# Optimization experiments

Hardware: AMD Instinct MI355X
Metric: run time of the kernel (lower is better)

Reference implementation:

```python
import jax, jax.numpy as jnp
import numpy as np

HEADS = 4
KS = 7          # neighborhood kernel size
EPS = 1e-5
C = 64
N, H, W = 8, 64, 64


def _gather_idx(L, k):
    # NATTEN-style neighborhood: window centered at pixel, shifted to stay in bounds.
    start = jnp.clip(jnp.arange(L) - k // 2, 0, L - k)            # [L]
    idx = start[:, None] + jnp.arange(k)                           # [L, k] absolute neighbor idx
    # relative-position-bias index: (query - neighbor) + (k-1) in [0, 2k-2]
    rel = (jnp.arange(L) - start)[:, None] + (k - 1) - jnp.arange(k)[None, :]  # [L, k]
    return idx, rel


def na2d(x, qkv_w, qkv_b, rpb, proj_w, proj_b):
    # x: [N, H, W, C] -> neighborhood attention with rel-pos bias
    n, h, w, c = x.shape
    hd = c // HEADS
    scale = hd ** -0.5
    qkv = (x @ qkv_w.T + qkv_b).reshape(n, h, w, 3, HEADS, hd)
    q = qkv[..., 0, :, :] * scale                                  # [n,h,w,heads,hd]
    k = qkv[..., 1, :, :]
    v = qkv[..., 2, :, :]
    idx_h, rel_h = _gather_idx(h, KS)
    idx_w, rel_w = _gather_idx(w, KS)
    # gather neighborhoods: [n, h, k, w, k, heads, hd]
    kg = k[:, idx_h][:, :, :, idx_w]
    vg = v[:, idx_h][:, :, :, idx_w]
    attn = jnp.einsum('nijhd,niajbhd->nijhab', q, kg)              # [n,h,w,heads,k,k]
    bias = rpb[:, rel_h, :]                                        # [heads, h, k, 2k-1]
    bias = jnp.take(bias, rel_w, axis=-1)                          # [heads, h, k, w, k]
    bias = jnp.transpose(bias, (1, 3, 0, 2, 4))                    # [h, w, heads, k, k]
    attn = attn + bias
    a = jax.nn.softmax(attn.reshape(n, h, w, HEADS, KS * KS), axis=-1).reshape(attn.shape)
    out = jnp.einsum('nijhab,niajbhd->nijhd', a, vg).reshape(n, h, w, c)
    return out @ proj_w.T + proj_b


def setup_inputs() -> dict:
    key = jax.random.key(0)
    ks = jax.random.split(key, 12)
    s = 0.02
    return {
        'x': jax.random.normal(ks[0], (N, C, H, W), jnp.float32),
        'gn_w': jnp.ones((C,), jnp.float32),
        'gn_b': jnp.zeros((C,), jnp.float32),
        'qkv_w': jax.random.normal(ks[1], (3 * C, C), jnp.float32) * s,
        'qkv_b': jnp.zeros((3 * C,), jnp.float32),
        'rpb': jax.random.normal(ks[2], (HEADS, 2 * KS - 1, 2 * KS - 1), jnp.float32) * s,
        'proj_w': jax.random.normal(ks[3], (C, C), jnp.float32) * s,
        'proj_b': jnp.zeros((C,), jnp.float32),
        'ln_w': jnp.ones((C,), jnp.float32),
        'ln_b': jnp.zeros((C,), jnp.float32),
        'fc1_w': jax.random.normal(ks[4], (4 * C, C), jnp.float32) * s,
        'fc1_b': jnp.zeros((4 * C,), jnp.float32),
        'fc2_w': jax.random.normal(ks[5], (C, 4 * C), jnp.float32) * s,
        'fc2_b': jnp.zeros((C,), jnp.float32),
    }


def reference(x, gn_w, gn_b, qkv_w, qkv_b, rpb, proj_w, proj_b,
              ln_w, ln_b, fc1_w, fc1_b, fc2_w, fc2_b):
    n, c, h, w = x.shape
    x1 = jnp.transpose(x, (0, 2, 3, 1))                            # residual, NHWC
    # GroupNorm(1, C): normalize over (C,H,W) per sample, per-channel affine
    mu = jnp.mean(x, axis=(1, 2, 3), keepdims=True)
    var = jnp.var(x, axis=(1, 2, 3), keepdims=True)
    xg = (x - mu) * jax.lax.rsqrt(var + EPS)
    xg = xg * gn_w[None, :, None, None] + gn_b[None, :, None, None]
    xg = jnp.transpose(xg, (0, 2, 3, 1))                           # NHWC
    y = na2d(xg, qkv_w, qkv_b, rpb, proj_w, proj_b) + x1           # [n,h,w,c]
    y = y.reshape(n, h * w, c)
    # LayerNorm over channels + MLP (GELU), residual
    mu2 = jnp.mean(y, axis=-1, keepdims=True)
    var2 = jnp.var(y, axis=-1, keepdims=True)
    yn = (y - mu2) * jax.lax.rsqrt(var2 + EPS) * ln_w + ln_b
    hdn = jax.nn.gelu(yn @ fc1_w.T + fc1_b, approximate=False)
    y = y + (hdn @ fc2_w.T + fc2_b)
    return jnp.transpose(y.reshape(n, h, w, c), (0, 3, 1, 2))      # back to NCHW
```

## Files before the change

kernel.cpp:

```cpp
#include <hip/hip_runtime.h>
#include <math.h>

#define NSAMP 8
#define CH 64
#define HH 64
#define WW 64
#define SPATIAL 4096
#define PER_SAMPLE 262144
#define NTOK 32768
#define NHEADS 4
#define HD 16
#define KS 7
#define EPS 1e-5f
#define QSCALE 0.25f

typedef __attribute__((ext_vector_type(8))) short short8;
typedef __attribute__((ext_vector_type(4))) float f32x4;

__device__ __forceinline__ unsigned short f2bf(float f) {
    unsigned u = __float_as_uint(f);
    u = u + 0x7fffu + ((u >> 16) & 1u);
    return (unsigned short)(u >> 16);
}
__device__ __forceinline__ unsigned pack2(float a, float b) {
    return (unsigned)f2bf(a) | ((unsigned)f2bf(b) << 16);
}
__device__ __forceinline__ float dot8_bf(uint4 u, const float* qv) {
    float s;
    s = __uint_as_float(u.x << 16) * qv[0];
    s = fmaf(__uint_as_float(u.x & 0xffff0000u), qv[1], s);
    s = fmaf(__uint_as_float(u.y << 16),         qv[2], s);
    s = fmaf(__uint_as_float(u.y & 0xffff0000u), qv[3], s);
    s = fmaf(__uint_as_float(u.z << 16),         qv[4], s);
    s = fmaf(__uint_as_float(u.z & 0xffff0000u), qv[5], s);
    s = fmaf(__uint_as_float(u.w << 16),         qv[6], s);
    s = fmaf(__uint_as_float(u.w & 0xffff0000u), qv[7], s);
    return s;
}
__device__ __forceinline__ void pv8_bf(uint4 u, float p, float* acc) {
    acc[0] = fmaf(p, __uint_as_float(u.x << 16),         acc[0]);
    acc[1] = fmaf(p, __uint_as_float(u.x & 0xffff0000u), acc[1]);
    acc[2] = fmaf(p, __uint_as_float(u.y << 16),         acc[2]);
    acc[3] = fmaf(p, __uint_as_float(u.y & 0xffff0000u), acc[3]);
    acc[4] = fmaf(p, __uint_as_float(u.z << 16),         acc[4]);
    acc[5] = fmaf(p, __uint_as_float(u.z & 0xffff0000u), acc[5]);
    acc[6] = fmaf(p, __uint_as_float(u.w << 16),         acc[6]);
    acc[7] = fmaf(p, __uint_as_float(u.w & 0xffff0000u), acc[7]);
}

__global__ __launch_bounds__(256) void k_statsprep(const float* __restrict__ x,
                                                   float* __restrict__ stats,
                                                   const float* __restrict__ qkv_w,
                                                   const float* __restrict__ fc1_w,
                                                   const float* __restrict__ fc2_w,
                                                   const float* __restrict__ proj_w,
                                                   unsigned short* __restrict__ wb) {
    int blk = blockIdx.x;
    if (blk >= 256) {
        int i = (blk - 256) * 256 + threadIdx.x;
        if (i < 12288)      wb[i] = f2bf(qkv_w[i]);
        else if (i < 28672) wb[i] = f2bf(fc1_w[i - 12288]);
        else if (i < 45056) wb[i] = f2bf(fc2_w[i - 28672]);
        else                wb[i] = f2bf(proj_w[i - 45056]);
        return;
    }
    int n = blk >> 5, chunk = blk & 31;
    const float4* p4 = (const float4*)(x + n * PER_SAMPLE + chunk * 8192);
    int t = threadIdx.x;
    float s1 = 0.f, s2 = 0.f;
#pragma unroll
    for (int i = 0; i < 8; i++) {
        float4 v = p4[t + i * 256];
        s1 += v.x + v.y + v.z + v.w;
        s2 += v.x * v.x + v.y * v.y + v.z * v.z + v.w * v.w;
    }
#pragma unroll
    for (int off = 1; off < 64; off <<= 1) {
        s1 += __shfl_xor(s1, off);
        s2 += __shfl_xor(s2, off);
    }
    __shared__ float r1[4], r2[4];
    int lane = t & 63, wv = t >> 6;
    if (lane == 0) { r1[wv] = s1; r2[wv] = s2; }
    __syncthreads();
    if (t == 0) {
        atomicAdd(&stats[n * 2 + 0], r1[0] + r1[1] + r1[2] + r1[3]);
        atomicAdd(&stats[n * 2 + 1], r2[0] + r2[1] + r2[2] + r2[3]);
    }
}

__global__ __launch_bounds__(256) void k_qkv(const float* __restrict__ x,
                                             const float* __restrict__ stats,
                                             const float* __restrict__ gn_w,
                                             const float* __restrict__ gn_b,
                                             const unsigned short* __restrict__ qkv_wb,
                                             const float* __restrict__ qkv_b,
                                             uint4* __restrict__ qb8,
                                             uint4* __restrict__ kvb8) {
    __shared__ __attribute__((aligned(16))) short fragA[2 * 2 * 64 * 8];
    __shared__ float obuf[4][16 * 33];
    int xcd = blockIdx.x & 7, idx = blockIdx.x >> 3;
    int half = idx & 1;
    int h = xcd * 8 + ((idx >> 1) & 7);
    int n = idx >> 4;
    int t = threadIdx.x, lane = t & 63;
    int g = __builtin_amdgcn_readfirstlane(t >> 6);
    int s0 = n * 4096 + h * 64 + half * 32;
    int nh = lane & 15, qd = lane >> 4;

    float mu = stats[2 * n] * (1.f / (float)PER_SAMPLE);
    float var = stats[2 * n + 1] * (1.f / (float)PER_SAMPLE) - mu * mu;
    float rstd = rsqrtf(var + EPS);

    {
        int tok32 = t & 31, cbq = t >> 5;
        const float* xp = x + n * PER_SAMPLE + h * 64 + half * 32 + tok32;
        float v[8];
#pragma unroll
        for (int i = 0; i < 8; i++) {
            int c = cbq * 8 + i;
            v[i] = (xp[(size_t)c * SPATIAL] - mu) * rstd * gn_w[c] + gn_b[c];
        }
        int kf = cbq >> 2, qsel = cbq & 3;
        uint4 p;
        p.x = pack2(v[0], v[1]);
        p.y = pack2(v[2], v[3]);
        p.z = pack2(v[4], v[5]);
        p.w = pack2(v[6], v[7]);
        *(uint4*)&fragA[(((tok32 >> 4) * 2 + kf) * 64 + (tok32 & 15) + (qsel << 4)) * 8] = p;
    }
    __syncthreads();

    short8 af[4];
#pragma unroll
    for (int mt = 0; mt < 2; mt++)
#pragma unroll
        for (int kf = 0; kf < 2; kf++)
            af[mt * 2 + kf] = *(const short8*)&fragA[((mt * 2 + kf) * 64 + lane) * 8];

    for (int nt = 0; nt < 3; nt++) {
        int n0 = g * 48 + nt * 16;
        const unsigned short* wp = qkv_wb + (size_t)(n0 + nh) * 64 + qd * 8;
        short8 b0 = *(const short8*)(wp);
        short8 b1 = *(const short8*)(wp + 32);
        float bias = qkv_b[n0 + nh];
        bool isq = (n0 < 64);
#pragma unroll
        for (int mt = 0; mt < 2; mt++) {
            f32x4 d = {0.f, 0.f, 0.f, 0.f};
            d = __builtin_amdgcn_mfma_f32_16x16x32_bf16(af[mt * 2 + 0], b0, d, 0, 0, 0);
            d = __builtin_amdgcn_mfma_f32_16x16x32_bf16(af[mt * 2 + 1], b1, d, 0, 0, 0);
#pragma unroll
            for (int r = 0; r < 4; r++) {
                float vv = d[r] + bias;
                if (isq) vv *= QSCALE;
                obuf[g][nh * 33 + mt * 16 + qd * 4 + r] = vv;
            }
        }
        __builtin_amdgcn_wave_barrier();
        {
            int tok = lane & 31, u = lane >> 5;
            uint4 p;
            p.x = pack2(obuf[g][(u * 8 + 0) * 33 + tok], obuf[g][(u * 8 + 1) * 33 + tok]);
            p.y = pack2(obuf[g][(u * 8 + 2) * 33 + tok], obuf[g][(u * 8 + 3) * 33 + tok]);
            p.z = pack2(obuf[g][(u * 8 + 4) * 33 + tok], obuf[g][(u * 8 + 5) * 33 + tok]);
            p.w = pack2(obuf[g][(u * 8 + 6) * 33 + tok], obuf[g][(u * 8 + 7) * 33 + tok]);
            int row = (n0 >> 3) + u;
            if (n0 < 64) qb8[(size_t)row * NTOK + s0 + tok] = p;
            else         kvb8[(size_t)(row - 8) * NTOK + s0 + tok] = p;
        }
        __builtin_amdgcn_wave_barrier();
    }
}

__global__ __launch_bounds__(256, 4) void k_fused(const uint4* __restrict__ qb8,
                                               const uint4* __restrict__ kvb8,
                                               const float* __restrict__ rpb,
                                               const unsigned short* __restrict__ proj_wb,
                                               const float* __restrict__ proj_b,
                                               const float* __restrict__ x,
                                               const float* __restrict__ ln_w,
                                               const float* __restrict__ ln_b,
                                               const unsigned short* __restrict__ fc1_wb,
                                               const float* __restrict__ fc1_b,
                                               const unsigned short* __restrict__ fc2_wb,
                                               const float* __restrict__ fc2_b,
                                               float* __restrict__ out) {
    __shared__ __attribute__((aligned(16))) short fragA[2 * 2 * 64 * 8];
    __shared__ __attribute__((aligned(16))) short lhA[2 * 8 * 64 * 8];
    __shared__ float obuf[4][16 * 33];
    __shared__ float red1[256], red2[256];
    int xcd = blockIdx.x & 7, idx = blockIdx.x >> 3;
    int tr = idx & 1;
    int tc = (idx >> 1) & 7;
    int n = idx >> 4;
    int h0 = xcd * 8 + tr * 4, c0 = tc * 8;
    int t = threadIdx.x, lane = t & 63;
    int g = __builtin_amdgcn_readfirstlane(t >> 6);
    int w2 = lane & 31;
    int dh = lane >> 5;
    int r = w2 >> 3, cseg = w2 & 7;
    int h = h0 + r, w = c0 + cseg;
    int tok = n * 4096 + h * 64 + w;
    int cb = 2 * g + dh;

    const float* xr = x + n * PER_SAMPLE + h * 64 + w;
    float xres[8];
#pragma unroll
    for (int i = 0; i < 8; i++)
        xres[i] = xr[(size_t)(cb * 8 + i) * SPATIAL];

    float q[8];
    {
        uint4 qa = qb8[(size_t)cb * NTOK + tok];
        q[0] = __uint_as_float(qa.x << 16); q[1] = __uint_as_float(qa.x & 0xffff0000u);
        q[2] = __uint_as_float(qa.y << 16); q[3] = __uint_as_float(qa.y & 0xffff0000u);
        q[4] = __uint_as_float(qa.z << 16); q[5] = __uint_as_float(qa.z & 0xffff0000u);
        q[6] = __uint_as_float(qa.w << 16); q[7] = __uint_as_float(qa.w & 0xffff0000u);
    }
    int sh = min(max(h - 3, 0), HH - KS);
    int sw = min(max(w - 3, 0), WW - KS);

    float sum = 0.f;
    float acc[8];
#pragma unroll
    for (int i = 0; i < 8; i++) acc[i] = 0.f;

#pragma unroll
    for (int a = 0; a < 7; a++) {
        int nb = n * 4096 + (sh + a) * 64 + sw;
        const float* rp = rpb + (g * 13 + (h - sh + 6 - a)) * 13 + (w - sw + 6);
        const uint4* kp = kvb8 + (size_t)cb * NTOK + nb;
        const uint4* vp = kvb8 + (size_t)(8 + cb) * NTOK + nb;
#pragma unroll
        for (int bb = 0; bb < 7; bb++) {
            uint4 kv = kp[bb];
            uint4 vv = vp[bb];
            float dhalf = dot8_bf(kv, q);
            float d = dhalf + __shfl_xor(dhalf, 32);
            d += rp[-bb];
            float e = __expf(d);
            sum += e;
            pv8_bf(vv, e, acc);
        }
    }
    float rs = 1.f / sum;

    {
        int kf = cb >> 2, qsel = cb & 3;
        uint4 p;
        p.x = pack2(acc[0] * rs, acc[1] * rs);
        p.y = pack2(acc[2] * rs, acc[3] * rs);
        p.z = pack2(acc[4] * rs, acc[5] * rs);
        p.w = pack2(acc[6] * rs, acc[7] * rs);
        *(uint4*)&fragA[(((w2 >> 4) * 2 + kf) * 64 + (w2 & 15) + (qsel << 4)) * 8] = p;
    }
    __syncthreads();

    int nh = lane & 15, qd = lane >> 4;
    float yreg[8];
    {
        short8 af[4];
#pragma unroll
        for (int mt = 0; mt < 2; mt++)
#pragma unroll
            for (int kf = 0; kf < 2; kf++)
                af[mt * 2 + kf] = *(const short8*)&fragA[((mt * 2 + kf) * 64 + lane) * 8];

        int n0 = g * 16;
        const unsigned short* wp = proj_wb + (size_t)(n0 + nh) * 64 + qd * 8;
        short8 b0 = *(const short8*)(wp);
        short8 b1 = *(const short8*)(wp + 32);
        float bias = proj_b[n0 + nh];
#pragma unroll
        for (int mt = 0; mt < 2; mt++) {
            f32x4 d = {0.f, 0.f, 0.f, 0.f};
            d = __builtin_amdgcn_mfma_f32_16x16x32_bf16(af[mt * 2 + 0], b0, d, 0, 0, 0);
            d = __builtin_amdgcn_mfma_f32_16x16x32_bf16(af[mt * 2 + 1], b1, d, 0, 0, 0);
#pragma unroll
            for (int r2 = 0; r2 < 4; r2++)
                obuf[g][nh * 33 + mt * 16 + qd * 4 + r2] = d[r2] + bias;
        }
        __builtin_amdgcn_wave_barrier();
#pragma unroll
        for (int i = 0; i < 8; i++)
            yreg[i] = obuf[g][(dh * 8 + i) * 33 + w2] + xres[i];
    }

    {
        float s1 = 0.f, s2 = 0.f;
#pragma unroll
        for (int i = 0; i < 8; i++) { s1 += yreg[i]; s2 += yreg[i] * yreg[i]; }
        red1[t] = s1;
        red2[t] = s2;
        __syncthreads();
        float m1 = 0.f, m2 = 0.f;
#pragma unroll
        for (int u = 0; u < 8; u++) { m1 += red1[u * 32 + w2]; m2 += red2[u * 32 + w2]; }
        float mu = m1 * (1.f / 64.f);
        float rstd = rsqrtf(m2 * (1.f / 64.f) - mu * mu + EPS);
        float v[8];
#pragma unroll
        for (int i = 0; i < 8; i++) {
            int c = cb * 8 + i;
            v[i] = (yreg[i] - mu) * rstd * ln_w[c] + ln_b[c];
        }
        int kf = cb >> 2, qsel = cb & 3;
        uint4 p;
        p.x = pack2(v[0], v[1]);
        p.y = pack2(v[2], v[3]);
        p.z = pack2(v[4], v[5]);
        p.w = pack2(v[6], v[7]);
        *(uint4*)&fragA[(((w2 >> 4) * 2 + kf) * 64 + (w2 & 15) + (qsel << 4)) * 8] = p;
    }
    __syncthreads();

    {
        short8 yf[4];
#pragma unroll
        for (int mt = 0; mt < 2; mt++)
#pragma unroll
            for (int kf = 0; kf < 2; kf++)
                yf[mt * 2 + kf] = *(const short8*)&fragA[((mt * 2 + kf) * 64 + lane) * 8];

#pragma unroll
        for (int nt = 0; nt < 4; nt++) {
            int n0f = g * 64 + nt * 16;
            const unsigned short* wp = fc1_wb + (size_t)(n0f + nh) * 64 + qd * 8;
            short8 b0 = *(const short8*)(wp);
            short8 b1 = *(const short8*)(wp + 32);
            float bias = fc1_b[n0f + nh];
            int j = n0f + nh;
            int kfA = j >> 5, q2 = (j >> 3) & 3, jb = j & 7;
#pragma unroll
            for (int mt = 0; mt < 2; mt++) {
                f32x4 d = {0.f, 0.f, 0.f, 0.f};
                d = __builtin_amdgcn_mfma_f32_16x16x32_bf16(yf[mt * 2 + 0], b0, d, 0, 0, 0);
                d = __builtin_amdgcn_mfma_f32_16x16x32_bf16(yf[mt * 2 + 1], b1, d, 0, 0, 0);
#pragma unroll
                for (int r2 = 0; r2 < 4; r2++) {
                    float hv = d[r2] + bias;
                    hv = 0.5f * hv * (1.f + erff(hv * 0.70710678118654752f));
                    lhA[((mt * 8 + kfA) * 64 + (qd * 4 + r2) + (q2 << 4)) * 8 + jb] = (short)f2bf(hv);
                }
            }
        }
    }
    __syncthreads();

    f32x4 acc2[2];
    acc2[0] = (f32x4){0.f, 0.f, 0.f, 0.f};
    acc2[1] = (f32x4){0.f, 0.f, 0.f, 0.f};
#pragma unroll
    for (int kfA = 0; kfA < 8; kfA++) {
        const unsigned short* wp = fc2_wb + (size_t)(g * 16 + nh) * 256 + kfA * 32 + qd * 8;
        short8 bb = *(const short8*)(wp);
#pragma unroll
        for (int mt = 0; mt < 2; mt++) {
            short8 a = *(const short8*)&lhA[((mt * 8 + kfA) * 64 + lane) * 8];
            acc2[mt] = __builtin_amdgcn_mfma_f32_16x16x32_bf16(a, bb, acc2[mt], 0, 0, 0);
        }
    }
#pragma unroll
    for (int mt = 0; mt < 2; mt++)
#pragma unroll
        for (int r2 = 0; r2 < 4; r2++)
            obuf[g][nh * 33 + mt * 16 + qd * 4 + r2] = acc2[mt][r2];
    __builtin_amdgcn_wave_barrier();
    float* op = out + (size_t)n * PER_SAMPLE + h * 64 + w;
#pragma unroll
    for (int i = 0; i < 8; i++) {
        int c = cb * 8 + i;
        op[(size_t)c * SPATIAL] = obuf[g][(dh * 8 + i) * 33 + w2] + fc2_b[c] + yreg[i];
    }
}

extern "C" void kernel_launch(void* const* d_in, const int* in_sizes, int n_in,
                              void* d_out, int out_size, void* d_ws, size_t ws_size,
                              hipStream_t stream) {
    const float* x      = (const float*)d_in[0];
    const float* gn_w   = (const float*)d_in[1];
    const float* gn_b   = (const float*)d_in[2];
    const float* qkv_w  = (const float*)d_in[3];
    const float* qkv_b  = (const float*)d_in[4];
    const float* rpb    = (const float*)d_in[5];
    const float* proj_w = (const float*)d_in[6];
    const float* proj_b = (const float*)d_in[7];
    const float* ln_w   = (const float*)d_in[8];
    const float* ln_b   = (const float*)d_in[9];
    const float* fc1_w  = (const float*)d_in[10];
    const float* fc1_b  = (const float*)d_in[11];
    const float* fc2_w  = (const float*)d_in[12];
    const float* fc2_b  = (const float*)d_in[13];
    float* out = (float*)d_out;

    float* ws    = (float*)d_ws;
    float* stats = ws;
    uint4* qb8   = (uint4*)(ws + 64);
    uint4* kvb8  = qb8 + (size_t)8 * NTOK;
    unsigned short* wb = (unsigned short*)(kvb8 + (size_t)16 * NTOK);
    unsigned short* qkv_wb  = wb;
    unsigned short* fc1_wb  = wb + 12288;
    unsigned short* fc2_wb  = wb + 28672;
    unsigned short* proj_wb = wb + 45056;

    hipMemsetAsync(stats, 0, 64, stream);
    k_statsprep<<<448, 256, 0, stream>>>(x, stats, qkv_w, fc1_w, fc2_w, proj_w, wb);
    k_qkv      <<<1024, 256, 0, stream>>>(x, stats, gn_w, gn_b, qkv_wb, qkv_b, qb8, kvb8);
    k_fused    <<<1024, 256, 0, stream>>>(qb8, kvb8, rpb, proj_wb, proj_b, x,
                                          ln_w, ln_b, fc1_wb, fc1_b, fc2_wb, fc2_b, out);
}
```

Measured before the change: 136.9 us.

## Stage K/V neighborhood halo tile in LDS before attention loop

Each block now cooperatively loads the 10x14 halo window of K and V (all 16 channel groups) into a shared-memory tile, then the 7x7 neighborhood loop reads K/V from LDS instead of global memory. This removes repeated global/L2 reads of overlapping neighborhoods across the block's 32 pixels. In exchange it adds a block barrier and raises LDS use to 40 KB, aliased with obuf, which may lower occupancy under the 4-blocks launch bound.

```diff
diff --git a/kernel.cpp b/kernel.cpp
--- a/kernel.cpp
+++ b/kernel.cpp
@@ -186,10 +186,14 @@
                                                const unsigned short* __restrict__ fc2_wb,
                                                const float* __restrict__ fc2_b,
                                                float* __restrict__ out) {
-    __shared__ __attribute__((aligned(16))) short fragA[2 * 2 * 64 * 8];
-    __shared__ __attribute__((aligned(16))) short lhA[2 * 8 * 64 * 8];
-    __shared__ float obuf[4][16 * 33];
-    __shared__ float red1[256], red2[256];
+    __shared__ __attribute__((aligned(16))) char smem[40960];
+    short* fragA = (short*)smem;
+    uint4* kvL   = (uint4*)(smem + 4096);
+    float (*obuf)[16 * 33] = (float(*)[16 * 33])(smem + 4096);
+    float* red1 = (float*)(smem + 12544);
+    float* red2 = (float*)(smem + 13568);
+    short* lhA  = (short*)(smem + 14592);
+
     int xcd = blockIdx.x & 7, idx = blockIdx.x >> 3;
     int tr = idx & 1;
     int tc = (idx >> 1) & 7;
@@ -204,6 +208,9 @@
     int tok = n * 4096 + h * 64 + w;
     int cb = 2 * g + dh;
 
+    int wr0 = max(h0 - 3, 0);
+    int wc0 = max(c0 - 3, 0);
+
     const float* xr = x + n * PER_SAMPLE + h * 64 + w;
     float xres[8];
 #pragma unroll
@@ -218,6 +225,22 @@
         q[4] = __uint_as_float(qa.z << 16); q[5] = __uint_as_float(qa.z & 0xffff0000u);
         q[6] = __uint_as_float(qa.w << 16); q[7] = __uint_as_float(qa.w & 0xffff0000u);
     }
+
+    {
+        int nb = n * 4096;
+#pragma unroll
+        for (int it = 0; it < 9; it++) {
+            int i = it * 256 + t;
+            if (i < 2240) {
+                int rr = i / 140, rem = i - rr * 140;
+                int swr = rem / 14, swc = rem - swr * 14;
+                int rowg = min(wr0 + swr, 63), colg = min(wc0 + swc, 63);
+                kvL[rr * 144 + rem] = kvb8[(size_t)rr * NTOK + nb + rowg * 64 + colg];
+            }
+        }
+    }
+    __syncthreads();
+
     int sh = min(max(h - 3, 0), HH - KS);
     int sw = min(max(w - 3, 0), WW - KS);
 
@@ -228,10 +251,10 @@
 
 #pragma unroll
     for (int a = 0; a < 7; a++) {
-        int nb = n * 4096 + (sh + a) * 64 + sw;
+        int wi_a = (sh - wr0 + a) * 14 + (sw - wc0);
         const float* rp = rpb + (g * 13 + (h - sh + 6 - a)) * 13 + (w - sw + 6);
-        const uint4* kp = kvb8 + (size_t)cb * NTOK + nb;
-        const uint4* vp = kvb8 + (size_t)(8 + cb) * NTOK + nb;
+        const uint4* kp = kvL + cb * 144 + wi_a;
+        const uint4* vp = kvL + (8 + cb) * 144 + wi_a;
 #pragma unroll
         for (int bb = 0; bb < 7; bb++) {
             uint4 kv = kp[bb];
```

New measurement: 130.2 us. 1.05x faster.
